# Kernel optimization log

Measured on AMD Instinct MI355X. Metric: run time of the kernel, lower is better.

The kernel has to match this reference:

```python
import jax, jax.numpy as jnp
import numpy as np

N = 50000     # nodes
E = 600000    # directed edges (avg degree 12)
F_IN = 128    # num_features
H = 128       # hidden_units
C = 16        # num_classes
G = 500       # graphs in batch


def setup_inputs() -> dict:
    key = jax.random.key(0)
    ks = jax.random.split(key, 6)
    x = jax.random.normal(ks[0], (N, F_IN), jnp.float32)
    edge_src = jax.random.randint(ks[1], (E,), 0, N, jnp.int32)
    edge_dst = jax.random.randint(ks[2], (E,), 0, N, jnp.int32)
    batch = jnp.sort(jax.random.randint(ks[3], (N,), 0, G, jnp.int32))
    W1 = jax.random.normal(ks[4], (F_IN, H), jnp.float32) / np.float32(np.sqrt(F_IN))
    b1 = jnp.zeros((H,), jnp.float32)
    W2 = jax.random.normal(ks[5], (H, C), jnp.float32) / np.float32(np.sqrt(H))
    b2 = jnp.zeros((C,), jnp.float32)
    return {"x": x, "W1": W1, "b1": b1, "W2": W2, "b2": b2,
            "edge_src": edge_src, "edge_dst": edge_dst, "batch": batch}


def _gcn_conv(x, W, b, src, dst, norm):
    # linear transform then normalized scatter-add aggregation (PyG GCNConv)
    h = x @ W                                   # [N, out]
    msg = h[src] * norm[:, None]                # [E+N, out]
    return jax.ops.segment_sum(msg, dst, num_segments=N) + b


def reference(x, W1, b1, W2, b2, edge_src, edge_dst, batch):
    # add self-loops
    loops = jnp.arange(N, dtype=edge_src.dtype)
    src = jnp.concatenate([edge_src, loops])
    dst = jnp.concatenate([edge_dst, loops])
    # symmetric normalization D^-1/2 A D^-1/2 (in-degree at targets)
    deg = jax.ops.segment_sum(jnp.ones_like(dst, jnp.float32), dst, num_segments=N)
    dis = jax.lax.rsqrt(deg)  # deg >= 1 because of self-loops
    norm = dis[src] * dis[dst]

    h = jax.nn.relu(_gcn_conv(x, W1, b1, src, dst, norm))
    h = _gcn_conv(h, W2, b2, src, dst, norm)

    # scatter_mean pooling over graphs
    counts = jax.ops.segment_sum(jnp.ones((N,), jnp.float32), batch, num_segments=G)
    pooled = jax.ops.segment_sum(h, batch, num_segments=G) / jnp.maximum(counts, 1.0)[:, None]
    return jax.nn.log_softmax(pooled, axis=1)
```

## Files before the change

kernel.cpp:

```cpp
#include <hip/hip_runtime.h>
#include <hip/hip_bf16.h>


#define NN 50000
#define EE 600000
#define FIN 128
#define HH 128
#define CC 16
#define GG 500
#define ETOT (EE + NN)
#define SBLK 196
#define WTS 140
#define CBLK ((EE + 255) / 256)
#define A1CAP 1024
#define A2CAP 2048

typedef unsigned short ushort_t;
typedef unsigned int uint_t;

typedef __attribute__((ext_vector_type(8))) short bf16x8;
typedef __attribute__((ext_vector_type(4))) ushort_t u16x4;
typedef __attribute__((ext_vector_type(4))) float f32x4;
typedef __attribute__((ext_vector_type(2))) float f32x2;

__device__ inline ushort_t f2bf(float f) {
    uint_t u = __float_as_uint(f);
    u = (u + 0x7FFFu + ((u >> 16) & 1u)) >> 16;
    return (ushort_t)u;
}
__device__ inline float bf2f(ushort_t b) {
    return __uint_as_float(((uint_t)b) << 16);
}
__device__ inline ushort_t f2h(float f) {
    _Float16 h = (_Float16)f; ushort_t u; __builtin_memcpy(&u, &h, 2); return u;
}
__device__ inline float h2f(ushort_t u) {
    _Float16 h; __builtin_memcpy(&h, &u, 2); return (float)h;
}

__global__ void init_kernel(int* cnt, float* pooled) {
    int i = blockIdx.x * blockDim.x + threadIdx.x;
    if (i < NN) cnt[i] = 0;
    if (i < GG * CC) pooled[i] = 0.0f;
}

__global__ __launch_bounds__(256) void cg1_kernel(const int* __restrict__ edge_dst,
                                                  int* __restrict__ cnt,
                                                  int* __restrict__ seq,
                                                  const float* __restrict__ x,
                                                  const float* __restrict__ W1,
                                                  unsigned char* __restrict__ hb8) {
    __shared__ ushort_t xs[64 * 136];
    __shared__ ushort_t wt[128 * WTS];
    if (blockIdx.x < CBLK) {
        int idx = blockIdx.x * 256 + threadIdx.x;
        if (idx < EE) seq[idx] = atomicAdd(&cnt[edge_dst[idx]], 1);
        return;
    }
    int t = threadIdx.x;
    int row0 = (blockIdx.x - CBLK) * 64;
    for (int i = 0; i < 8; i++) {
        int slot = t + i * 256;
        int r = slot >> 5, k4 = slot & 31;
        int gr = row0 + r;
        float4 v = (gr < NN) ? ((const float4*)x)[gr * 32 + k4]
                             : make_float4(0.f, 0.f, 0.f, 0.f);
        u16x4 bv = { f2bf(v.x), f2bf(v.y), f2bf(v.z), f2bf(v.w) };
        *(u16x4*)(&xs[r * 136 + k4 * 4]) = bv;
    }
    for (int i = 0; i < 16; i++) {
        int idx = t + i * 256;
        int c = idx & 127, k4 = idx >> 7;
        u16x4 bv = { f2bf(W1[(4 * k4 + 0) * HH + c]),
                     f2bf(W1[(4 * k4 + 1) * HH + c]),
                     f2bf(W1[(4 * k4 + 2) * HH + c]),
                     f2bf(W1[(4 * k4 + 3) * HH + c]) };
        *(u16x4*)(&wt[c * WTS + k4 * 4]) = bv;
    }
    __syncthreads();

    int wave = t >> 6, lane = t & 63;
    int m = lane & 15, quad = lane >> 4;
    f32x4 acc[8];
    for (int ct = 0; ct < 8; ct++) acc[ct] = (f32x4)(0.0f);
    for (int ko = 0; ko < 4; ko++) {
        bf16x8 a = *(const bf16x8*)(&xs[(16 * wave + m) * 136 + ko * 32 + quad * 8]);
        for (int ct = 0; ct < 8; ct++) {
            bf16x8 b = *(const bf16x8*)(&wt[(ct * 16 + m) * WTS + ko * 32 + quad * 8]);
            acc[ct] = __builtin_amdgcn_mfma_f32_16x16x32_bf16(a, b, acc[ct], 0, 0, 0);
        }
    }
    for (int ct = 0; ct < 8; ct++) {
        int gcol = ct * 16 + m;
        for (int r = 0; r < 4; r++) {
            int grow = row0 + wave * 16 + quad * 4 + r;
            if (grow < NN) {
                int p = __builtin_amdgcn_cvt_pk_fp8_f32(acc[ct][r], 0.0f, 0, false);
                hb8[(size_t)grow * HH + gcol] = (unsigned char)(p & 0xFF);
            }
        }
    }
}

__device__ inline int block_excl_scan(int v, int t, int* total) {
    __shared__ int wsum[4];
    int lane = t & 63, wv = t >> 6;
    int inc = v;
    for (int off = 1; off < 64; off <<= 1) {
        int n = __shfl_up(inc, off);
        if (lane >= off) inc += n;
    }
    if (lane == 63) wsum[wv] = inc;
    __syncthreads();
    int off_w = 0;
    for (int w = 0; w < wv; w++) off_w += wsum[w];
    *total = wsum[0] + wsum[1] + wsum[2] + wsum[3];
    return off_w + inc - v;
}

__global__ __launch_bounds__(256) void scanA_kernel(const int* __restrict__ cnt,
                                                    int* __restrict__ rowptr,
                                                    float* __restrict__ dis,
                                                    int* __restrict__ bsum,
                                                    const int* __restrict__ batch,
                                                    int* __restrict__ gstart) {
    int t = threadIdx.x;
    int i = blockIdx.x * 256 + t;
    int d = 0;
    if (i < NN) {
        d = cnt[i] + 1;
        dis[i] = rsqrtf((float)d);
        int b = batch[i];
        int bp = (i == 0) ? -1 : batch[i - 1];
        for (int g = bp + 1; g <= b; ++g) gstart[g] = i;
        if (i == NN - 1) {
            for (int g = b + 1; g <= GG; ++g) gstart[g] = NN;
        }
    }
    int total;
    int excl = block_excl_scan(d, t, &total);
    if (i < NN) rowptr[i] = excl;
    if (t == 0) bsum[blockIdx.x] = total;
}

__global__ __launch_bounds__(256) void scanBC_kernel(int* __restrict__ rowptr,
                                                     const int* __restrict__ bsum) {
    __shared__ int sb[256];
    int t = threadIdx.x;
    int v = (t < SBLK) ? bsum[t] : 0;
    int total;
    int ex = block_excl_scan(v, t, &total);
    sb[t] = ex;
    __syncthreads();
    int myoff = sb[blockIdx.x];
    int i = blockIdx.x * 256 + t;
    if (i < NN) rowptr[i] += myoff;
    if (blockIdx.x == 0 && t == 0) rowptr[NN] = ETOT;
}

__global__ void fill_kernel(const int* __restrict__ edge_src,
                            const int* __restrict__ edge_dst,
                            const float* __restrict__ dis,
                            const int* __restrict__ rowptr,
                            const int* __restrict__ seq,
                            uint_t* __restrict__ csr) {
    int idx = blockIdx.x * blockDim.x + threadIdx.x;
    if (idx < EE) {
        int s = edge_src[idx], d = edge_dst[idx];
        csr[rowptr[d] + seq[idx]] = (uint_t)s | ((uint_t)f2h(dis[s]) << 16);
    } else if (idx < ETOT) {
        int n = idx - EE;
        csr[rowptr[n + 1] - 1] = (uint_t)n | ((uint_t)f2h(dis[n]) << 16);
    }
}

__global__ __launch_bounds__(256) void agg1f_kernel(const unsigned char* __restrict__ hb8,
                                                    const int* __restrict__ rowptr,
                                                    const uint_t* __restrict__ csr,
                                                    const float* __restrict__ dis,
                                                    const float* __restrict__ b1,
                                                    const float* __restrict__ W2,
                                                    ushort_t* __restrict__ h2b) {
    __shared__ uint_t w2s[8 * 132];
    __shared__ uint_t ecsr[A1CAP];
    int t = threadIdx.x;
    int node0 = blockIdx.x * 4;
    int wave = t >> 6, lane = t & 63;
    int node = node0 + wave;
    int slot = lane >> 3, sub = lane & 7;
    int wbeg = rowptr[node0];
    int wcap = rowptr[node0 + 4];
    int e0 = rowptr[node], e1 = rowptr[node + 1];
    float dn = dis[node];
    {
        const float2* W2v = (const float2*)W2;
        for (int i = t; i < HH * 8; i += 256) {
            int k = i >> 3, sl = i & 7;
            float2 wv = W2v[i];
            w2s[(k >> 4) * 132 + (k & 15) * 8 + sl] =
                (uint_t)f2bf(wv.x) | ((uint_t)f2bf(wv.y) << 16);
        }
    }
    int wlen = min(wcap - wbeg, A1CAP);
    for (int i = t; i < wlen; i += 256) ecsr[i] = csr[wbeg + i];
    __syncthreads();
    int wend = wbeg + wlen;

    float acc[16];
    for (int j = 0; j < 16; j++) acc[j] = 0.0f;
    for (int e = e0 + slot; e < e1; e += 16) {
        uint_t ent0;
        if (e < wend) ent0 = ecsr[e - wbeg]; else ent0 = csr[e];
        bool has2 = (e + 8) < e1;
        uint_t ent1 = ent0;
        if (has2) {
            if (e + 8 < wend) ent1 = ecsr[e + 8 - wbeg]; else ent1 = csr[e + 8];
        }
        uint4 hv0 = *(const uint4*)(hb8 + (size_t)(ent0 & 0xFFFFu) * HH + sub * 16);
        uint4 hv1 = has2 ? *(const uint4*)(hb8 + (size_t)(ent1 & 0xFFFFu) * HH + sub * 16)
                         : make_uint4(0, 0, 0, 0);
        float w0 = h2f((ushort_t)(ent0 >> 16));
        uint_t words0[4] = { hv0.x, hv0.y, hv0.z, hv0.w };
        for (int q = 0; q < 4; q++) {
            f32x2 lo = __builtin_amdgcn_cvt_pk_f32_fp8(words0[q], false);
            f32x2 hi = __builtin_amdgcn_cvt_pk_f32_fp8(words0[q], true);
            acc[q * 4 + 0] += w0 * lo[0];
            acc[q * 4 + 1] += w0 * lo[1];
            acc[q * 4 + 2] += w0 * hi[0];
            acc[q * 4 + 3] += w0 * hi[1];
        }
        if (has2) {
            float w1 = h2f((ushort_t)(ent1 >> 16));
            uint_t words1[4] = { hv1.x, hv1.y, hv1.z, hv1.w };
            for (int q = 0; q < 4; q++) {
                f32x2 lo = __builtin_amdgcn_cvt_pk_f32_fp8(words1[q], false);
                f32x2 hi = __builtin_amdgcn_cvt_pk_f32_fp8(words1[q], true);
                acc[q * 4 + 0] += w1 * lo[0];
                acc[q * 4 + 1] += w1 * lo[1];
                acc[q * 4 + 2] += w1 * hi[0];
                acc[q * 4 + 3] += w1 * hi[1];
            }
        }
    }
    for (int j = 0; j < 16; j++) {
        acc[j] += __shfl_xor(acc[j], 8);
        acc[j] += __shfl_xor(acc[j], 16);
        acc[j] += __shfl_xor(acc[j], 32);
    }
    const float4* b1v = (const float4*)(b1 + sub * 16);
    float4 bb[4] = { b1v[0], b1v[1], b1v[2], b1v[3] };
    const float* bbf = (const float*)bb;
    float p0 = 0.0f, p1 = 0.0f;
    int wbase = sub * 132 + slot;
    for (int j = 0; j < 16; j++) {
        float h = fmaxf(dn * acc[j] + bbf[j], 0.0f);
        uint_t w = w2s[wbase + j * 8];
        p0 += h * __uint_as_float(w << 16);
        p1 += h * __uint_as_float(w & 0xFFFF0000u);
    }
    p0 += __shfl_xor(p0, 1); p0 += __shfl_xor(p0, 2); p0 += __shfl_xor(p0, 4);
    p1 += __shfl_xor(p1, 1); p1 += __shfl_xor(p1, 2); p1 += __shfl_xor(p1, 4);
    if (sub == 0) {
        uint_t pk = (uint_t)f2bf(p0) | ((uint_t)f2bf(p1) << 16);
        *(uint_t*)(h2b + (size_t)node * CC + 2 * slot) = pk;
    }
}

__global__ __launch_bounds__(1024) void agg2pool_kernel(const ushort_t* __restrict__ h2b,
                                                        const int* __restrict__ rowptr,
                                                        const uint_t* __restrict__ csr,
                                                        const float* __restrict__ dis,
                                                        const float* __restrict__ b2,
                                                        const int* __restrict__ batch,
                                                        float* __restrict__ pooled) {
    __shared__ float vals[16][16];
    __shared__ int gid[16];
    __shared__ uint_t ecsr[A2CAP];
    int wave = threadIdx.x >> 6, lane = threadIdx.x & 63;
    int node0 = blockIdx.x * 16;
    int node = node0 + wave;
    int slot = lane >> 3, sub = lane & 7;
    int wbeg = rowptr[node0];
    int wcap = rowptr[node0 + 16];
    int e0 = rowptr[node], e1 = rowptr[node + 1];
    float dn = dis[node];
    int   bg = batch[node];
    float b20 = b2[2 * sub], b21 = b2[2 * sub + 1];
    int wlen = min(wcap - wbeg, A2CAP);
    for (int i = threadIdx.x; i < wlen; i += 1024) ecsr[i] = csr[wbeg + i];
    __syncthreads();
    int wend = wbeg + wlen;

    float a0 = 0.0f, a1 = 0.0f;
    for (int e = e0 + slot; e < e1; e += 16) {
        uint_t ent0;
        if (e < wend) ent0 = ecsr[e - wbeg]; else ent0 = csr[e];
        bool has2 = (e + 8) < e1;
        uint_t ent1 = ent0;
        if (has2) {
            if (e + 8 < wend) ent1 = ecsr[e + 8 - wbeg]; else ent1 = csr[e + 8];
        }
        uint_t p0 = *(const uint_t*)(h2b + (size_t)(ent0 & 0xFFFFu) * CC + sub * 2);
        uint_t p1 = has2 ? *(const uint_t*)(h2b + (size_t)(ent1 & 0xFFFFu) * CC + sub * 2) : 0;
        float w0 = h2f((ushort_t)(ent0 >> 16));
        a0 += w0 * bf2f((ushort_t)(p0 & 0xFFFFu));
        a1 += w0 * bf2f((ushort_t)(p0 >> 16));
        if (has2) {
            float w1 = h2f((ushort_t)(ent1 >> 16));
            a0 += w1 * bf2f((ushort_t)(p1 & 0xFFFFu));
            a1 += w1 * bf2f((ushort_t)(p1 >> 16));
        }
    }
    a0 += __shfl_xor(a0, 8); a0 += __shfl_xor(a0, 16); a0 += __shfl_xor(a0, 32);
    a1 += __shfl_xor(a1, 8); a1 += __shfl_xor(a1, 16); a1 += __shfl_xor(a1, 32);
    if (slot == 0) {
        vals[wave][2 * sub]     = a0 * dn + b20;
        vals[wave][2 * sub + 1] = a1 * dn + b21;
        if (sub == 0) gid[wave] = bg;
    }
    __syncthreads();
    if (threadIdx.x < 16) {
        int c = threadIdx.x;
        float run = 0.0f;
        for (int i = 0; i < 16; i++) {
            run += vals[i][c];
            if (i == 15 || gid[i + 1] != gid[i]) {
                atomicAdd(&pooled[gid[i] * CC + c], run);
                run = 0.0f;
            }
        }
    }
}

__global__ void lsm_kernel(const float* __restrict__ pooled,
                           const int* __restrict__ gstart,
                           float* __restrict__ out) {
    int idx = blockIdx.x * blockDim.x + threadIdx.x;
    int g = idx >> 4, c = idx & 15;
    if (g >= GG) return;
    float cnt = (float)(gstart[g + 1] - gstart[g]);
    float v = pooled[g * CC + c] / fmaxf(cnt, 1.0f);
    float m = v;
    for (int off = 8; off >= 1; off >>= 1) m = fmaxf(m, __shfl_xor(m, off, 16));
    float s = expf(v - m);
    for (int off = 8; off >= 1; off >>= 1) s += __shfl_xor(s, off, 16);
    out[g * CC + c] = v - m - logf(s);
}

extern "C" void kernel_launch(void* const* d_in, const int* in_sizes, int n_in,
                              void* d_out, int out_size, void* d_ws, size_t ws_size,
                              hipStream_t stream) {
    const float* x  = (const float*)d_in[0];
    const float* W1 = (const float*)d_in[1];
    const float* b1 = (const float*)d_in[2];
    const float* W2 = (const float*)d_in[3];
    const float* b2 = (const float*)d_in[4];
    const int* edge_src = (const int*)d_in[5];
    const int* edge_dst = (const int*)d_in[6];
    const int* batch    = (const int*)d_in[7];
    float* out = (float*)d_out;

    char* ws = (char*)d_ws;
    size_t off = 0;
    auto alloc = [&](size_t bytes) {
        void* p = ws + off;
        off += (bytes + 255) & ~size_t(255);
        return p;
    };
    int*   cnt     = (int*)  alloc(NN * 4);
    float* dis     = (float*)alloc(NN * 4);
    int*   rowptr  = (int*)  alloc((NN + 1) * 4);
    int*   seq     = (int*)  alloc(EE * 4);
    int*   bsum    = (int*)  alloc(SBLK * 4);
    uint_t* csr    = (uint_t*)alloc((size_t)ETOT * 4);
    unsigned char* hb8 = (unsigned char*)alloc((size_t)NN * HH);
    ushort_t* h2b  = (ushort_t*)alloc((size_t)NN * CC * 2);
    float* pooled  = (float*)alloc(GG * CC * 4);
    int*   gstart  = (int*)  alloc((GG + 1) * 4);

    const int B = 256;
    init_kernel<<<(NN + B - 1) / B, B, 0, stream>>>(cnt, pooled);
    cg1_kernel<<<CBLK + (NN + 63) / 64, B, 0, stream>>>(edge_dst, cnt, seq, x, W1, hb8);
    scanA_kernel<<<SBLK, B, 0, stream>>>(cnt, rowptr, dis, bsum, batch, gstart);
    scanBC_kernel<<<SBLK, B, 0, stream>>>(rowptr, bsum);
    fill_kernel<<<(ETOT + B - 1) / B, B, 0, stream>>>(edge_src, edge_dst, dis,
                                                      rowptr, seq, csr);
    agg1f_kernel<<<NN / 4, B, 0, stream>>>(hb8, rowptr, csr, dis, b1, W2, h2b);
    agg2pool_kernel<<<NN / 16, 1024, 0, stream>>>(h2b, rowptr, csr, dis, b2, batch, pooled);
    lsm_kernel<<<(GG * CC + B - 1) / B, B, 0, stream>>>(pooled, gstart, out);
}
```

Baseline: 195.3 us.

## Merge scan kernels into single-block scan and fuse log-softmax via last-block

Replaces the two-kernel block scan with one single-block 1024-thread scan that also zeroes the pooled buffer, and folds the final log-softmax into the aggregation kernel using an atomic done-counter so the last block finishes the output. It also adds an occupancy hint to agg1f. The aim is to cut two kernel launches and their inter-kernel gaps. The price is a serial single-CU scan over 50k nodes, with about 49 sequential elements per thread, plus a grid-wide atomic and fence at the end of agg2.

```diff
diff --git a/kernel.cpp b/kernel.cpp
--- a/kernel.cpp
+++ b/kernel.cpp
@@ -9,7 +9,6 @@
 #define CC 16
 #define GG 500
 #define ETOT (EE + NN)
-#define SBLK 196
 #define WTS 140
 #define CBLK ((EE + 255) / 256)
 #define A1CAP 1024
@@ -38,10 +37,10 @@
     _Float16 h; __builtin_memcpy(&h, &u, 2); return (float)h;
 }
 
-__global__ void init_kernel(int* cnt, float* pooled) {
+__global__ void init_kernel(int* cnt, int* done) {
     int i = blockIdx.x * blockDim.x + threadIdx.x;
     if (i < NN) cnt[i] = 0;
-    if (i < GG * CC) pooled[i] = 0.0f;
+    if (i == 0) *done = 0;
 }
 
 __global__ __launch_bounds__(256) void cg1_kernel(const int* __restrict__ edge_dst,
@@ -102,60 +101,57 @@
     }
 }
 
-__device__ inline int block_excl_scan(int v, int t, int* total) {
-    __shared__ int wsum[4];
+__global__ __launch_bounds__(1024) void scanF_kernel(const int* __restrict__ cnt,
+                                                     int* __restrict__ rowptr,
+                                                     float* __restrict__ dis,
+                                                     const int* __restrict__ batch,
+                                                     int* __restrict__ gstart,
+                                                     float* __restrict__ pooled) {
+    __shared__ int wpart[16];
+    int t = threadIdx.x;
+    const int CH = (NN + 1023) / 1024;
+    int base = t * CH;
+    int s = 0;
+    for (int j = 0; j < CH; j++) {
+        int i = base + j;
+        if (i < NN) s += cnt[i] + 1;
+    }
     int lane = t & 63, wv = t >> 6;
-    int inc = v;
+    int inc = s;
     for (int off = 1; off < 64; off <<= 1) {
         int n = __shfl_up(inc, off);
         if (lane >= off) inc += n;
     }
-    if (lane == 63) wsum[wv] = inc;
-    __syncthreads();
-    int off_w = 0;
-    for (int w = 0; w < wv; w++) off_w += wsum[w];
-    *total = wsum[0] + wsum[1] + wsum[2] + wsum[3];
-    return off_w + inc - v;
-}
-
-__global__ __launch_bounds__(256) void scanA_kernel(const int* __restrict__ cnt,
-                                                    int* __restrict__ rowptr,
-                                                    float* __restrict__ dis,
-                                                    int* __restrict__ bsum,
-                                                    const int* __restrict__ batch,
-                                                    int* __restrict__ gstart) {
-    int t = threadIdx.x;
-    int i = blockIdx.x * 256 + t;
-    int d = 0;
-    if (i < NN) {
-        d = cnt[i] + 1;
-        dis[i] = rsqrtf((float)d);
-        int b = batch[i];
-        int bp = (i == 0) ? -1 : batch[i - 1];
-        for (int g = bp + 1; g <= b; ++g) gstart[g] = i;
-        if (i == NN - 1) {
-            for (int g = b + 1; g <= GG; ++g) gstart[g] = NN;
-        }
-    }
-    int total;
-    int excl = block_excl_scan(d, t, &total);
-    if (i < NN) rowptr[i] = excl;
-    if (t == 0) bsum[blockIdx.x] = total;
-}
-
-__global__ __launch_bounds__(256) void scanBC_kernel(int* __restrict__ rowptr,
-                                                     const int* __restrict__ bsum) {
-    __shared__ int sb[256];
-    int t = threadIdx.x;
-    int v = (t < SBLK) ? bsum[t] : 0;
-    int total;
-    int ex = block_excl_scan(v, t, &total);
-    sb[t] = ex;
-    __syncthreads();
-    int myoff = sb[blockIdx.x];
-    int i = blockIdx.x * 256 + t;
-    if (i < NN) rowptr[i] += myoff;
-    if (blockIdx.x == 0 && t == 0) rowptr[NN] = ETOT;
+    if (lane == 63) wpart[wv] = inc;
+    __syncthreads();
+    if (t < 16) {
+        int v = wpart[t];
+        int in2 = v;
+        for (int off = 1; off < 16; off <<= 1) {
+            int n = __shfl_up(in2, off);
+            if (t >= off) in2 += n;
+        }
+        wpart[t] = in2 - v;
+    }
+    __syncthreads();
+    int run = wpart[wv] + inc - s;
+    for (int j = 0; j < CH; j++) {
+        int i = base + j;
+        if (i < NN) {
+            int d = cnt[i] + 1;
+            rowptr[i] = run;
+            run += d;
+            dis[i] = rsqrtf((float)d);
+            int b = batch[i];
+            int bp = (i == 0) ? -1 : batch[i - 1];
+            for (int g = bp + 1; g <= b; ++g) gstart[g] = i;
+            if (i == NN - 1) {
+                for (int g = b + 1; g <= GG; ++g) gstart[g] = NN;
+            }
+        }
+    }
+    if (t == 0) rowptr[NN] = ETOT;
+    for (int i = t; i < GG * CC; i += 1024) pooled[i] = 0.0f;
 }
 
 __global__ void fill_kernel(const int* __restrict__ edge_src,
@@ -174,13 +170,13 @@
     }
 }
 
-__global__ __launch_bounds__(256) void agg1f_kernel(const unsigned char* __restrict__ hb8,
-                                                    const int* __restrict__ rowptr,
-                                                    const uint_t* __restrict__ csr,
-                                                    const float* __restrict__ dis,
-                                                    const float* __restrict__ b1,
-                                                    const float* __restrict__ W2,
-                                                    ushort_t* __restrict__ h2b) {
+__global__ __launch_bounds__(256, 4) void agg1f_kernel(const unsigned char* __restrict__ hb8,
+                                                       const int* __restrict__ rowptr,
+                                                       const uint_t* __restrict__ csr,
+                                                       const float* __restrict__ dis,
+                                                       const float* __restrict__ b1,
+                                                       const float* __restrict__ W2,
+                                                       ushort_t* __restrict__ h2b) {
     __shared__ uint_t w2s[8 * 132];
     __shared__ uint_t ecsr[A1CAP];
     int t = threadIdx.x;
@@ -266,16 +262,20 @@
     }
 }
 
-__global__ __launch_bounds__(1024) void agg2pool_kernel(const ushort_t* __restrict__ h2b,
-                                                        const int* __restrict__ rowptr,
-                                                        const uint_t* __restrict__ csr,
-                                                        const float* __restrict__ dis,
-                                                        const float* __restrict__ b2,
-                                                        const int* __restrict__ batch,
-                                                        float* __restrict__ pooled) {
+__global__ __launch_bounds__(1024) void agg2pl_kernel(const ushort_t* __restrict__ h2b,
+                                                      const int* __restrict__ rowptr,
+                                                      const uint_t* __restrict__ csr,
+                                                      const float* __restrict__ dis,
+                                                      const float* __restrict__ b2,
+                                                      const int* __restrict__ batch,
+                                                      float* __restrict__ pooled,
+                                                      const int* __restrict__ gstart,
+                                                      int* __restrict__ done,
+                                                      float* __restrict__ out) {
     __shared__ float vals[16][16];
     __shared__ int gid[16];
     __shared__ uint_t ecsr[A2CAP];
+    __shared__ int amlast;
     int wave = threadIdx.x >> 6, lane = threadIdx.x & 63;
     int node0 = blockIdx.x * 16;
     int node = node0 + wave;
@@ -330,21 +330,26 @@
             }
         }
     }
-}
-
-__global__ void lsm_kernel(const float* __restrict__ pooled,
-                           const int* __restrict__ gstart,
-                           float* __restrict__ out) {
-    int idx = blockIdx.x * blockDim.x + threadIdx.x;
-    int g = idx >> 4, c = idx & 15;
-    if (g >= GG) return;
-    float cnt = (float)(gstart[g + 1] - gstart[g]);
-    float v = pooled[g * CC + c] / fmaxf(cnt, 1.0f);
-    float m = v;
-    for (int off = 8; off >= 1; off >>= 1) m = fmaxf(m, __shfl_xor(m, off, 16));
-    float s = expf(v - m);
-    for (int off = 8; off >= 1; off >>= 1) s += __shfl_xor(s, off, 16);
-    out[g * CC + c] = v - m - logf(s);
+    __syncthreads();
+    if (threadIdx.x == 0) {
+        __threadfence();
+        int old = atomicAdd(done, 1);
+        amlast = (old == (int)gridDim.x - 1);
+    }
+    __syncthreads();
+    if (amlast) {
+        __threadfence();
+        for (int idx = threadIdx.x; idx < GG * CC; idx += 1024) {
+            int g = idx >> 4;
+            float cntg = (float)(gstart[g + 1] - gstart[g]);
+            float v = pooled[idx] / fmaxf(cntg, 1.0f);
+            float m = v;
+            for (int off = 8; off >= 1; off >>= 1) m = fmaxf(m, __shfl_xor(m, off, 16));
+            float s = expf(v - m);
+            for (int off = 8; off >= 1; off >>= 1) s += __shfl_xor(s, off, 16);
+            out[idx] = v - m - logf(s);
+        }
+    }
 }
 
 extern "C" void kernel_launch(void* const* d_in, const int* in_sizes, int n_in,
@@ -371,21 +376,20 @@
     float* dis     = (float*)alloc(NN * 4);
     int*   rowptr  = (int*)  alloc((NN + 1) * 4);
     int*   seq     = (int*)  alloc(EE * 4);
-    int*   bsum    = (int*)  alloc(SBLK * 4);
     uint_t* csr    = (uint_t*)alloc((size_t)ETOT * 4);
     unsigned char* hb8 = (unsigned char*)alloc((size_t)NN * HH);
     ushort_t* h2b  = (ushort_t*)alloc((size_t)NN * CC * 2);
     float* pooled  = (float*)alloc(GG * CC * 4);
     int*   gstart  = (int*)  alloc((GG + 1) * 4);
+    int*   done    = (int*)  alloc(256);
 
     const int B = 256;
-    init_kernel<<<(NN + B - 1) / B, B, 0, stream>>>(cnt, pooled);
+    init_kernel<<<(NN + B - 1) / B, B, 0, stream>>>(cnt, done);
     cg1_kernel<<<CBLK + (NN + 63) / 64, B, 0, stream>>>(edge_dst, cnt, seq, x, W1, hb8);
-    scanA_kernel<<<SBLK, B, 0, stream>>>(cnt, rowptr, dis, bsum, batch, gstart);
-    scanBC_kernel<<<SBLK, B, 0, stream>>>(rowptr, bsum);
+    scanF_kernel<<<1, 1024, 0, stream>>>(cnt, rowptr, dis, batch, gstart, pooled);
     fill_kernel<<<(ETOT + B - 1) / B, B, 0, stream>>>(edge_src, edge_dst, dis,
                                                       rowptr, seq, csr);
     agg1f_kernel<<<NN / 4, B, 0, stream>>>(hb8, rowptr, csr, dis, b1, W2, h2b);
-    agg2pool_kernel<<<NN / 16, 1024, 0, stream>>>(h2b, rowptr, csr, dis, b2, batch, pooled);
-    lsm_kernel<<<(GG * CC + B - 1) / B, B, 0, stream>>>(pooled, gstart, out);
-}
+    agg2pl_kernel<<<NN / 16, 1024, 0, stream>>>(h2b, rowptr, csr, dis, b2, batch,
+                                                pooled, gstart, done, out);
+}
```

New measurement: 451.2 us. 131% more time.
